# Kernel optimization log

Hardware: AMD Instinct MI355X
Metric: run time of the kernel (lower is better)

The kernel has to match this reference:

```python
import jax, jax.numpy as jnp
import numpy as np

# Two atom types (e.g. H and O) with per-atom auxiliary basis dims 16 and 48.
N_H, D_H = 40000, 16   # number of H-type atoms, basis functions per H atom
N_O, D_O = 20000, 48   # number of O-type atoms, basis functions per O atom
C = 32                 # channels
EPS = 1e-6


def _psd(key, d):
    # Stand-in for the pyscf per-atom overlap matrix: symmetric PSD.
    a = jax.random.normal(key, (d, d), dtype=jnp.float32)
    return a @ a.T / d + 0.5 * jnp.eye(d, dtype=jnp.float32)


def setup_inputs() -> dict:
    key = jax.random.key(0)
    k1, k2, k3 = jax.random.split(key, 3)
    n_total = N_H * D_H + N_O * D_O  # 1,600,000 basis rows
    x = jax.random.normal(k1, (n_total, C), dtype=jnp.float32)
    S_H = _psd(k2, D_H)
    S_O = _psd(k3, D_O)
    # Index arrays equivalent to the boolean atomic_number_masks: all basis
    # functions of H-type atoms first, then O-type (contiguous per atom).
    idx_H = jnp.arange(N_H * D_H, dtype=jnp.int32)
    idx_O = jnp.arange(N_O * D_O, dtype=jnp.int32) + N_H * D_H
    return {"x": x, "S_H": S_H, "S_O": S_O, "idx_H": idx_H, "idx_O": idx_O}


def _l2_function_norm_atom(y, S):
    # y: [n_atoms, d, C], S: [d, d]
    # norm_{a,c} = sum_{i,j} S_ij * y_{a,i,c} * y_{a,j,c}
    norm = jnp.einsum('ij,aic,ajc->ac', S, y, y)
    norm = jnp.sqrt(norm)[:, None, :]  # [n_atoms, 1, C], matches unsqueeze(1)
    return y / (norm + EPS)


def reference(x, S_H, S_O, idx_H, idx_O):
    # H-type atoms: gather -> per-atom bilinear L2 norm -> scatter back
    y = x[idx_H].reshape(N_H, D_H, C)
    x = x.at[idx_H].set(_l2_function_norm_atom(y, S_H).reshape(-1, C))
    # O-type atoms (reads the updated x, as in the sequential torch loop;
    # index sets are disjoint so order does not change the result)
    y = x[idx_O].reshape(N_O, D_O, C)
    x = x.at[idx_O].set(_l2_function_norm_atom(y, S_O).reshape(-1, C))
    return x
```

## Files before the change

kernel.cpp:

```cpp
#include <hip/hip_runtime.h>
#include <cstdint>
#include <cstddef>

#define NH 40000
#define DH 16
#define NO 20000
#define DO_ 48
#define CH 32

#define OBLOCKS (NO / 8)
#define HBLOCKS (NH / 16)

typedef float f32x2 __attribute__((ext_vector_type(2)));

__global__ __launch_bounds__(256) void l2norm_fused(
    const float* __restrict__ x, float* __restrict__ out,
    const float* __restrict__ SH, const float* __restrict__ SO) {
  const int b = blockIdx.x;
  const int idx = b >> 1;

  if ((b & 1) == 0) {
    const int c  = threadIdx.x & 31;
    const int al = threadIdx.x >> 5;
    const int atom = idx * 8 + al;
    const size_t base =
        (size_t)NH * DH * CH + (size_t)atom * DO_ * CH + (size_t)c;

    float yv[DO_];
#pragma unroll
    for (int i = 0; i < DO_; ++i) yv[i] = x[base + (size_t)i * CH];

    float acc = 0.f;
#pragma unroll
    for (int i = 0; i < DO_; ++i) {
      float s = 0.f;
#pragma unroll
      for (int j = 0; j < i; ++j)
        s = fmaf(SO[i * DO_ + j], yv[j], s);
      const float t = fmaf(SO[i * DO_ + i], yv[i], 2.f * s);
      acc = fmaf(t, yv[i], acc);
    }

    const float inv = 1.f / (sqrtf(acc) + 1e-6f);
#pragma unroll
    for (int i = 0; i < DO_; ++i)
      __builtin_nontemporal_store(yv[i] * inv, &out[base + (size_t)i * CH]);
  } else {
    const f32x2* __restrict__ x2 = (const f32x2*)x;
    f32x2* __restrict__ o2 = (f32x2*)out;
    const int cp = threadIdx.x & 15;
    const int al = threadIdx.x >> 4;
    const int atom = idx * 16 + al;
    const size_t base = (size_t)atom * DH * 16 + (size_t)cp;

    f32x2 yv[DH];
#pragma unroll
    for (int i = 0; i < DH; ++i) yv[i] = x2[base + (size_t)i * 16];

    float ax = 0.f, ay = 0.f;
#pragma unroll
    for (int i = 0; i < DH; ++i) {
      float sx = 0.f, sy = 0.f;
#pragma unroll
      for (int j = 0; j < i; ++j) {
        const float s = SH[i * DH + j];
        sx = fmaf(s, yv[j].x, sx);
        sy = fmaf(s, yv[j].y, sy);
      }
      const float sd = SH[i * DH + i];
      const float tx = fmaf(sd, yv[i].x, 2.f * sx);
      const float ty = fmaf(sd, yv[i].y, 2.f * sy);
      ax = fmaf(tx, yv[i].x, ax);
      ay = fmaf(ty, yv[i].y, ay);
    }

    const float ix = 1.f / (sqrtf(ax) + 1e-6f);
    const float iy = 1.f / (sqrtf(ay) + 1e-6f);

#pragma unroll
    for (int i = 0; i < DH; ++i) {
      f32x2 r;
      r.x = yv[i].x * ix;
      r.y = yv[i].y * iy;
      __builtin_nontemporal_store(r, &o2[base + (size_t)i * 16]);
    }
  }
}

extern "C" void kernel_launch(void* const* d_in, const int* in_sizes, int n_in,
                              void* d_out, int out_size, void* d_ws, size_t ws_size,
                              hipStream_t stream) {
  const float* x  = (const float*)d_in[0];
  const float* SH = (const float*)d_in[1];
  const float* SO = (const float*)d_in[2];
  float* out = (float*)d_out;

  l2norm_fused<<<OBLOCKS + HBLOCKS, 256, 0, stream>>>(x, out, SH, SO);
}
```

Before: 352.9 us.

## Stage atom chunks through LDS with vectorized loads and tile the O bilinear form

Each block now copies its contiguous chunk of x into shared memory with 16-byte vector loads, then each thread reads its atom's channel column from LDS. The 48x48 O-type quadratic form is computed in 16x16 tiles so only 32 values sit in registers instead of 48, which lowers register pressure and should raise occupancy. H blocks now handle 8 atoms each, interleaved 1:2 with O blocks. In exchange every block uses 48 KB of LDS regardless of type and needs a barrier, which may cap how many blocks fit per CU.

```diff
diff --git a/kernel.cpp b/kernel.cpp
--- a/kernel.cpp
+++ b/kernel.cpp
@@ -8,82 +8,108 @@
 #define DO_ 48
 #define CH 32
 
-#define OBLOCKS (NO / 8)
-#define HBLOCKS (NH / 16)
+typedef float f32x4 __attribute__((ext_vector_type(4)));
 
-typedef float f32x2 __attribute__((ext_vector_type(2)));
+#define XO_BASE ((size_t)NH * DH * CH)
+#define OATOMS 8
+#define HATOMS 8
+#define OBLOCKS (NO / OATOMS)
+#define HBLOCKS (NH / HATOMS)
+#define OCHUNK (OATOMS * DO_ * CH)
+#define HCHUNK (HATOMS * DH * CH)
 
 __global__ __launch_bounds__(256) void l2norm_fused(
     const float* __restrict__ x, float* __restrict__ out,
     const float* __restrict__ SH, const float* __restrict__ SO) {
+  __shared__ __align__(16) float lds[OCHUNK];
+  const int t = threadIdx.x;
   const int b = blockIdx.x;
-  const int idx = b >> 1;
+  const int r = b % 3;
+  const int q = b / 3;
 
-  if ((b & 1) == 0) {
-    const int c  = threadIdx.x & 31;
-    const int al = threadIdx.x >> 5;
-    const int atom = idx * 8 + al;
-    const size_t base =
-        (size_t)NH * DH * CH + (size_t)atom * DO_ * CH + (size_t)c;
+  if (r == 0) {
+    const size_t gbase = XO_BASE + (size_t)q * OCHUNK;
+    const f32x4* __restrict__ g4 = (const f32x4*)(x + gbase);
+    f32x4* lds4 = (f32x4*)lds;
+#pragma unroll
+    for (int k = 0; k < OCHUNK / 4 / 256; ++k)
+      lds4[k * 256 + t] = g4[k * 256 + t];
+    __syncthreads();
 
-    float yv[DO_];
+    const int a = t >> 5, c = t & 31;
+    const int abase = a * (DO_ * CH) + c;
+
+    float acc = 0.f;
+    float yi[16], yj[16];
 #pragma unroll
-    for (int i = 0; i < DO_; ++i) yv[i] = x[base + (size_t)i * CH];
+    for (int ti = 0; ti < 3; ++ti) {
+#pragma unroll
+      for (int k = 0; k < 16; ++k)
+        yi[k] = lds[abase + (ti * 16 + k) * CH];
+#pragma unroll
+      for (int i = 0; i < 16; ++i) {
+        float s = 0.f;
+#pragma unroll
+        for (int j = 0; j < i; ++j)
+          s = fmaf(SO[(ti * 16 + i) * DO_ + (ti * 16 + j)], yi[j], s);
+        const float sd = SO[(ti * 16 + i) * DO_ + (ti * 16 + i)];
+        acc = fmaf(fmaf(sd, yi[i], 2.f * s), yi[i], acc);
+      }
+#pragma unroll
+      for (int tj = 0; tj < ti; ++tj) {
+#pragma unroll
+        for (int k = 0; k < 16; ++k)
+          yj[k] = lds[abase + (tj * 16 + k) * CH];
+#pragma unroll
+        for (int i = 0; i < 16; ++i) {
+          float s = 0.f;
+#pragma unroll
+          for (int j = 0; j < 16; ++j)
+            s = fmaf(SO[(ti * 16 + i) * DO_ + (tj * 16 + j)], yj[j], s);
+          acc = fmaf(2.f * s, yi[i], acc);
+        }
+      }
+    }
+
+    const float inv = 1.f / (sqrtf(acc) + 1e-6f);
+    float* o = out + gbase;
+#pragma unroll
+    for (int i = 0; i < DO_; ++i)
+      __builtin_nontemporal_store(lds[abase + i * CH] * inv,
+                                  &o[abase + i * CH]);
+  } else {
+    const int idx = q * 2 + (r - 1);
+    const size_t gbase = (size_t)idx * HCHUNK;
+    const f32x4* __restrict__ g4 = (const f32x4*)(x + gbase);
+    f32x4* lds4 = (f32x4*)lds;
+#pragma unroll
+    for (int k = 0; k < HCHUNK / 4 / 256; ++k)
+      lds4[k * 256 + t] = g4[k * 256 + t];
+    __syncthreads();
+
+    const int a = t >> 5, c = t & 31;
+    const int abase = a * (DH * CH) + c;
+
+    float yi[DH];
+#pragma unroll
+    for (int k = 0; k < DH; ++k)
+      yi[k] = lds[abase + k * CH];
 
     float acc = 0.f;
 #pragma unroll
-    for (int i = 0; i < DO_; ++i) {
+    for (int i = 0; i < DH; ++i) {
       float s = 0.f;
 #pragma unroll
       for (int j = 0; j < i; ++j)
-        s = fmaf(SO[i * DO_ + j], yv[j], s);
-      const float t = fmaf(SO[i * DO_ + i], yv[i], 2.f * s);
-      acc = fmaf(t, yv[i], acc);
+        s = fmaf(SH[i * DH + j], yi[j], s);
+      acc = fmaf(fmaf(SH[i * DH + i], yi[i], 2.f * s), yi[i], acc);
     }
 
     const float inv = 1.f / (sqrtf(acc) + 1e-6f);
+    float* o = out + gbase;
 #pragma unroll
-    for (int i = 0; i < DO_; ++i)
-      __builtin_nontemporal_store(yv[i] * inv, &out[base + (size_t)i * CH]);
-  } else {
-    const f32x2* __restrict__ x2 = (const f32x2*)x;
-    f32x2* __restrict__ o2 = (f32x2*)out;
-    const int cp = threadIdx.x & 15;
-    const int al = threadIdx.x >> 4;
-    const int atom = idx * 16 + al;
-    const size_t base = (size_t)atom * DH * 16 + (size_t)cp;
-
-    f32x2 yv[DH];
-#pragma unroll
-    for (int i = 0; i < DH; ++i) yv[i] = x2[base + (size_t)i * 16];
-
-    float ax = 0.f, ay = 0.f;
-#pragma unroll
-    for (int i = 0; i < DH; ++i) {
-      float sx = 0.f, sy = 0.f;
-#pragma unroll
-      for (int j = 0; j < i; ++j) {
-        const float s = SH[i * DH + j];
-        sx = fmaf(s, yv[j].x, sx);
-        sy = fmaf(s, yv[j].y, sy);
-      }
-      const float sd = SH[i * DH + i];
-      const float tx = fmaf(sd, yv[i].x, 2.f * sx);
-      const float ty = fmaf(sd, yv[i].y, 2.f * sy);
-      ax = fmaf(tx, yv[i].x, ax);
-      ay = fmaf(ty, yv[i].y, ay);
-    }
-
-    const float ix = 1.f / (sqrtf(ax) + 1e-6f);
-    const float iy = 1.f / (sqrtf(ay) + 1e-6f);
-
-#pragma unroll
-    for (int i = 0; i < DH; ++i) {
-      f32x2 r;
-      r.x = yv[i].x * ix;
-      r.y = yv[i].y * iy;
-      __builtin_nontemporal_store(r, &o2[base + (size_t)i * 16]);
-    }
+    for (int i = 0; i < DH; ++i)
+      __builtin_nontemporal_store(yi[i] * inv, &o[abase + i * CH]);
   }
 }
 
```

Result: slower. 371.7 us (+5.3%).
